# Performance work log

Hardware: AMD Instinct MI355X
Metric: run time of the kernel (lower is better)

The kernel has to match this reference:

```python
import jax, jax.numpy as jnp
import numpy as np

LN_EPS = 1e-5

def _ln(x, g, b):
    # LayerNorm over last dim; torch normalized_shape=[1,H] on [B,1,H] reduces to this
    mu = jnp.mean(x, axis=-1, keepdims=True)
    var = jnp.var(x, axis=-1, keepdims=True)
    return (x - mu) * jax.lax.rsqrt(var + LN_EPS) * g + b


def setup_inputs() -> dict:
    key = jax.random.key(0)
    B, T, D, H = 32, 2048, 512, 128
    ks = jax.random.split(key, 10)
    stdu = 1.0 / np.sqrt(H)
    u = lambda k, sh: jax.random.uniform(k, sh, jnp.float32, -stdu, stdu)
    return {
        "x": jax.random.normal(ks[0], (B, T, D), jnp.float32),
        "W_f": u(ks[1], (D, H)), "W_i": u(ks[2], (D, H)),
        "W_o": u(ks[3], (D, H)), "W_c": u(ks[4], (D, H)),
        "U_f": u(ks[5], (H, H)), "U_i": u(ks[6], (H, H)),
        "U_o": u(ks[7], (H, H)), "U_c": u(ks[8], (H, H)),
        "b_f": jnp.ones((H,), jnp.float32),
        "b_i": jnp.zeros((H,), jnp.float32),
        "b_o": jnp.zeros((H,), jnp.float32),
        "b_c": jnp.zeros((H,), jnp.float32),
        "ln_f_g": jnp.ones((H,), jnp.float32), "ln_f_b": jnp.zeros((H,), jnp.float32),
        "ln_i_g": jnp.ones((H,), jnp.float32), "ln_i_b": jnp.zeros((H,), jnp.float32),
        "ln_o_g": jnp.ones((H,), jnp.float32), "ln_o_b": jnp.zeros((H,), jnp.float32),
        "ln_c_g": jnp.ones((H,), jnp.float32), "ln_c_b": jnp.zeros((H,), jnp.float32),
        "h0": jnp.zeros((B, H), jnp.float32),
        "c0": jnp.zeros((B, H), jnp.float32),
        "zoneout_mask": jax.random.randint(ks[9], (T,), 0, 2, jnp.int32),
    }


def reference(x, W_f, W_i, W_o, W_c, U_f, U_i, U_o, U_c,
              b_f, b_i, b_o, b_c,
              ln_f_g, ln_f_b, ln_i_g, ln_i_b, ln_o_g, ln_o_b, ln_c_g, ln_c_b,
              h0, c0, zoneout_mask):
    xs = jnp.swapaxes(x, 0, 1)                       # [T, B, D]
    m = zoneout_mask.astype(x.dtype)[:, None, None]  # [T, 1, 1] zoneout indicator

    def step(carry, inp):
        h, c = carry
        x_t, mt = inp
        f = jax.nn.sigmoid(_ln(x_t @ W_f + h @ U_f + b_f, ln_f_g, ln_f_b))
        i = jax.nn.sigmoid(_ln(x_t @ W_i + h @ U_i + b_i, ln_i_g, ln_i_b))
        o = jax.nn.sigmoid(_ln(x_t @ W_o + h @ U_o + b_o, ln_o_g, ln_o_b))
        ch = jax.nn.sigmoid(_ln(x_t @ W_c + h @ U_c + b_c, ln_c_g, ln_c_b))
        c_new = mt * c + (1.0 - mt) * (f * c + i * ch)
        # NOTE: source applies sigmoid (not tanh) to the cell state
        h_new = mt * h + (1.0 - mt) * (o * jax.nn.sigmoid(c_new))
        return (h_new, c_new), h_new

    (h_T, c_T), out_seq = jax.lax.scan(step, (h0, c0), (xs, m))
    return jnp.swapaxes(out_seq, 0, 1), h_T          # [B, T, H], [B, H]
```

## Files before the change

### kernel.cpp

```cpp
#include <hip/hip_runtime.h>
#include <hip/hip_bf16.h>

#define Bx 32
#define Tt 2048
#define Dd 512
#define Hh 128

typedef __attribute__((ext_vector_type(8))) short short8;
typedef __attribute__((ext_vector_type(4))) float f32x4;

static __device__ __forceinline__ short f2bf(float f) {
    __hip_bfloat16 h = __float2bfloat16(f);
    return *reinterpret_cast<short*>(&h);
}
static __device__ __forceinline__ float sigm(float x) {
    return 1.f / (1.f + __expf(-x));
}

template<int CTRL>
static __device__ __forceinline__ float dpp_add(float v) {
    return v + __int_as_float(__builtin_amdgcn_update_dpp(
        0, __float_as_int(v), CTRL, 0xF, 0xF, true));
}
static __device__ __forceinline__ float swz_xor16_add(float v) {
    return v + __int_as_float(__builtin_amdgcn_ds_swizzle(__float_as_int(v), 0x401F));
}

#define BARRIER_LGKM() asm volatile("s_waitcnt lgkmcnt(0)\n\ts_barrier" ::: "memory")

typedef __attribute__((address_space(1))) const void gas_void;
typedef __attribute__((address_space(3))) void las_void;
static __device__ __forceinline__ void gl_lds16(const float* g, float* l) {
    __builtin_amdgcn_global_load_lds((gas_void*)g, (las_void*)l, 16, 0, 0);
}

__global__ __launch_bounds__(512, 2) void gemm_xw_mfma(
    const float* __restrict__ X,
    const float* __restrict__ W0, const float* __restrict__ W1,
    const float* __restrict__ W2, const float* __restrict__ W3,
    float* __restrict__ G)
{
    __shared__ __align__(16) short As[128][40];
    __shared__ __align__(16) short Bs[512][40];

    const int tid  = threadIdx.x;
    const int m0   = blockIdx.x * 128;
    const int lane = tid & 63;
    const int w    = tid >> 6;
    const int wr   = w >> 2, wc = w & 3;
    const int l15  = lane & 15, kb = lane >> 4;

    const int bn   = tid;
    const int gate = bn >> 7;
    const int j    = bn & 127;
    const float* __restrict__ Wg = (gate == 0) ? W0 : (gate == 1) ? W1 : (gate == 2) ? W2 : W3;

    const int am = tid >> 2;
    const int ak = (tid & 3) * 8;

    f32x4 acc[4][8];
    #pragma unroll
    for (int mt = 0; mt < 4; ++mt)
        #pragma unroll
        for (int nt = 0; nt < 8; ++nt)
            acc[mt][nt] = (f32x4){0.f, 0.f, 0.f, 0.f};

    for (int k0 = 0; k0 < Dd; k0 += 32) {
        {
            const float4* xp = (const float4*)&X[(size_t)(m0 + am) * Dd + k0 + ak];
            float4 v0 = xp[0], v1 = xp[1];
            short8 s;
            s[0] = f2bf(v0.x); s[1] = f2bf(v0.y); s[2] = f2bf(v0.z); s[3] = f2bf(v0.w);
            s[4] = f2bf(v1.x); s[5] = f2bf(v1.y); s[6] = f2bf(v1.z); s[7] = f2bf(v1.w);
            *(short8*)&As[am][ak] = s;
        }
        #pragma unroll
        for (int rc = 0; rc < 4; ++rc) {
            float v[8];
            #pragma unroll
            for (int r = 0; r < 8; ++r)
                v[r] = Wg[(size_t)(k0 + rc * 8 + r) * Hh + j];
            short8 s;
            #pragma unroll
            for (int r = 0; r < 8; ++r) s[r] = f2bf(v[r]);
            *(short8*)&Bs[bn][rc * 8] = s;
        }
        __syncthreads();

        short8 a[4], b[8];
        #pragma unroll
        for (int mt = 0; mt < 4; ++mt)
            a[mt] = *(const short8*)&As[wr * 64 + mt * 16 + l15][kb * 8];
        #pragma unroll
        for (int nt = 0; nt < 8; ++nt)
            b[nt] = *(const short8*)&Bs[wc * 128 + nt * 16 + l15][kb * 8];
        #pragma unroll
        for (int mt = 0; mt < 4; ++mt)
            #pragma unroll
            for (int nt = 0; nt < 8; ++nt)
                acc[mt][nt] = __builtin_amdgcn_mfma_f32_16x16x32_bf16(a[mt], b[nt], acc[mt][nt], 0, 0, 0);
        __syncthreads();
    }

    #pragma unroll
    for (int mt = 0; mt < 4; ++mt)
        #pragma unroll
        for (int nt = 0; nt < 8; ++nt)
            #pragma unroll
            for (int r = 0; r < 4; ++r)
                G[(size_t)(m0 + wr * 64 + mt * 16 + kb * 4 + r) * 512 + wc * 128 + nt * 16 + l15]
                    = acc[mt][nt][r];
}

__global__ __launch_bounds__(512, 1) void lstm_scan_mfma(
    const float* __restrict__ G,
    const float* __restrict__ Uf, const float* __restrict__ Ui,
    const float* __restrict__ Uo, const float* __restrict__ Uc,
    const float* __restrict__ bf_, const float* __restrict__ bi_,
    const float* __restrict__ bo_, const float* __restrict__ bc_,
    const float* __restrict__ lnfg, const float* __restrict__ lnfb,
    const float* __restrict__ lnig, const float* __restrict__ lnib,
    const float* __restrict__ lnog, const float* __restrict__ lnob,
    const float* __restrict__ lncg, const float* __restrict__ lncb,
    const float* __restrict__ h0, const float* __restrict__ c0,
    const int* __restrict__ zmask,
    float* __restrict__ out, float* __restrict__ hT)
{
    const int tid  = threadIdx.x;
    const int lane = tid & 63;
    const int w    = tid >> 6;
    const int b0   = blockIdx.x * 4;

    __shared__ __align__(16) short Ap[16 * 136];
    __shared__ __align__(16) float ST[512 * 10];
    __shared__ __align__(16) float Pan[2 * 4 * 4 * 512];
    __shared__ unsigned short act[Tt];
    __shared__ int wsum[8], wpre[8];
    __shared__ int nact_sh;

    const int gate = w >> 1;
    const float* __restrict__ Ug = (gate == 0) ? Uf : (gate == 1) ? Ui : (gate == 2) ? Uo : Uc;
    const int n0  = w * 64;
    const int l15 = lane & 15;
    const int kb  = lane >> 4;

    short8 bfr[4][4];
    #pragma unroll
    for (int nt = 0; nt < 4; ++nt) {
        const int jloc = (n0 & 127) + nt * 16 + l15;
        #pragma unroll
        for (int ks = 0; ks < 4; ++ks) {
            short8 v;
            #pragma unroll
            for (int r = 0; r < 8; ++r)
                v[r] = f2bf(Ug[(ks * 32 + kb * 8 + r) * Hh + jloc]);
            bfr[nt][ks] = v;
        }
    }

    const int rowL = tid >> 5;
    const int bL   = rowL >> 2;
    const int gL   = rowL & 3;
    const int cl   = tid & 31;
    const float* lnGp = (gL == 0) ? lnfg : (gL == 1) ? lnig : (gL == 2) ? lnog : lncg;
    const float* lnBp = (gL == 0) ? lnfb : (gL == 1) ? lnib : (gL == 2) ? lnob : lncb;
    const float* bgp  = (gL == 0) ? bf_  : (gL == 1) ? bi_  : (gL == 2) ? bo_  : bc_;
    float lgam[4], lbet[4], lbias[4];
    #pragma unroll
    for (int kk = 0; kk < 4; ++kk) {
        const int jc = cl + 32 * kk;
        lgam[kk] = lnGp[jc]; lbet[kk] = lnBp[jc]; lbias[kk] = bgp[jc];
    }

    const int ob = tid >> 7;
    const int oj = tid & 127;
    float hval = h0[(b0 + ob) * Hh + oj];
    float cval = c0[(b0 + ob) * Hh + oj];

    for (int i = tid; i < 16 * 136; i += 512) Ap[i] = 0;
    __syncthreads();
    Ap[ob * 136 + oj] = f2bf(hval);

    {
        const int base_t = tid * 4;
        const int f0 = (zmask[base_t] == 0), f1 = (zmask[base_t + 1] == 0);
        const int f2 = (zmask[base_t + 2] == 0), f3 = (zmask[base_t + 3] == 0);
        const int cnt = f0 + f1 + f2 + f3;
        int scan = cnt;
        #pragma unroll
        for (int off = 1; off <= 32; off <<= 1) {
            int v = __shfl_up(scan, off);
            if (lane >= off) scan += v;
        }
        if (lane == 63) wsum[w] = scan;
        __syncthreads();
        if (tid == 0) {
            int s = 0;
            #pragma unroll
            for (int i = 0; i < 8; ++i) { wpre[i] = s; s += wsum[i]; }
            nact_sh = s;
        }
        __syncthreads();
        int pos = wpre[w] + scan - cnt;
        if (f0) act[pos++] = (unsigned short)(base_t);
        if (f1) act[pos++] = (unsigned short)(base_t + 1);
        if (f2) act[pos++] = (unsigned short)(base_t + 2);
        if (f3) act[pos++] = (unsigned short)(base_t + 3);
    }
    __syncthreads();
    const int nact = nact_sh;

    auto stage_panel = [&](int kp, int buf) {
        #pragma unroll
        for (int si = 0; si < 2; ++si) {
            const int s    = w * 2 + si;
            const int slot = s >> 2;
            const int bb   = s & 3;
            const int kidx = kp + slot;
            if (kidx < nact) {
                const int tt = (int)act[kidx];
                const float* src = &G[((size_t)(b0 + bb) * Tt + tt) * 512];
                float* dst = &Pan[((buf * 4 + slot) * 4 + bb) * 512];
                gl_lds16(src + lane * 4, dst);
                gl_lds16(src + 256 + lane * 4, dst + 256);
            }
        }
    };

    int cur = 0;
    stage_panel(0, 0);
    asm volatile("s_waitcnt vmcnt(0)" ::: "memory");
    __syncthreads();

    auto lstm_step = [&](int kidx, int slot) {
        const int t_ = (int)act[kidx];

        float Gv[4][4];
        #pragma unroll
        for (int nt = 0; nt < 4; ++nt)
            #pragma unroll
            for (int r = 0; r < 4; ++r)
                Gv[nt][r] = Pan[((cur * 4 + slot) * 4 + r) * 512 + n0 + nt * 16 + l15];

        short8 a0 = *(const short8*)&Ap[l15 * 136 +  0 + kb * 8];
        short8 a1 = *(const short8*)&Ap[l15 * 136 + 32 + kb * 8];
        short8 a2 = *(const short8*)&Ap[l15 * 136 + 64 + kb * 8];
        short8 a3 = *(const short8*)&Ap[l15 * 136 + 96 + kb * 8];

        f32x4 C0 = {Gv[0][0], Gv[0][1], Gv[0][2], Gv[0][3]};
        f32x4 C1 = {Gv[1][0], Gv[1][1], Gv[1][2], Gv[1][3]};
        f32x4 C2 = {Gv[2][0], Gv[2][1], Gv[2][2], Gv[2][3]};
        f32x4 C3 = {Gv[3][0], Gv[3][1], Gv[3][2], Gv[3][3]};

        C0 = __builtin_amdgcn_mfma_f32_16x16x32_bf16(a0, bfr[0][0], C0, 0, 0, 0);
        C1 = __builtin_amdgcn_mfma_f32_16x16x32_bf16(a0, bfr[1][0], C1, 0, 0, 0);
        C2 = __builtin_amdgcn_mfma_f32_16x16x32_bf16(a0, bfr[2][0], C2, 0, 0, 0);
        C3 = __builtin_amdgcn_mfma_f32_16x16x32_bf16(a0, bfr[3][0], C3, 0, 0, 0);
        C0 = __builtin_amdgcn_mfma_f32_16x16x32_bf16(a1, bfr[0][1], C0, 0, 0, 0);
        C1 = __builtin_amdgcn_mfma_f32_16x16x32_bf16(a1, bfr[1][1], C1, 0, 0, 0);
        C2 = __builtin_amdgcn_mfma_f32_16x16x32_bf16(a1, bfr[2][1], C2, 0, 0, 0);
        C3 = __builtin_amdgcn_mfma_f32_16x16x32_bf16(a1, bfr[3][1], C3, 0, 0, 0);
        C0 = __builtin_amdgcn_mfma_f32_16x16x32_bf16(a2, bfr[0][2], C0, 0, 0, 0);
        C1 = __builtin_amdgcn_mfma_f32_16x16x32_bf16(a2, bfr[1][2], C1, 0, 0, 0);
        C2 = __builtin_amdgcn_mfma_f32_16x16x32_bf16(a2, bfr[2][2], C2, 0, 0, 0);
        C3 = __builtin_amdgcn_mfma_f32_16x16x32_bf16(a2, bfr[3][2], C3, 0, 0, 0);
        C0 = __builtin_amdgcn_mfma_f32_16x16x32_bf16(a3, bfr[0][3], C0, 0, 0, 0);
        C1 = __builtin_amdgcn_mfma_f32_16x16x32_bf16(a3, bfr[1][3], C1, 0, 0, 0);
        C2 = __builtin_amdgcn_mfma_f32_16x16x32_bf16(a3, bfr[2][3], C2, 0, 0, 0);
        C3 = __builtin_amdgcn_mfma_f32_16x16x32_bf16(a3, bfr[3][3], C3, 0, 0, 0);

        if (lane < 16) {
            *(float2*)&ST[(n0 +  0 + l15) * 10]     = make_float2(C0[0], C0[1]);
            *(float2*)&ST[(n0 +  0 + l15) * 10 + 2] = make_float2(C0[2], C0[3]);
            *(float2*)&ST[(n0 + 16 + l15) * 10]     = make_float2(C1[0], C1[1]);
            *(float2*)&ST[(n0 + 16 + l15) * 10 + 2] = make_float2(C1[2], C1[3]);
            *(float2*)&ST[(n0 + 32 + l15) * 10]     = make_float2(C2[0], C2[1]);
            *(float2*)&ST[(n0 + 32 + l15) * 10 + 2] = make_float2(C2[2], C2[3]);
            *(float2*)&ST[(n0 + 48 + l15) * 10]     = make_float2(C3[0], C3[1]);
            *(float2*)&ST[(n0 + 48 + l15) * 10 + 2] = make_float2(C3[2], C3[3]);
        }
        BARRIER_LGKM();

        float s0_ = ST[(gL * 128 + cl +  0) * 10 + bL] + lbias[0];
        float s1_ = ST[(gL * 128 + cl + 32) * 10 + bL] + lbias[1];
        float s2_ = ST[(gL * 128 + cl + 64) * 10 + bL] + lbias[2];
        float s3_ = ST[(gL * 128 + cl + 96) * 10 + bL] + lbias[3];
        float sm = (s0_ + s1_) + (s2_ + s3_);
        float sq = s0_ * s0_ + s1_ * s1_ + s2_ * s2_ + s3_ * s3_;
        sm = dpp_add<0xB1>(sm);  sq = dpp_add<0xB1>(sq);
        sm = dpp_add<0x4E>(sm);  sq = dpp_add<0x4E>(sq);
        sm = dpp_add<0x124>(sm); sq = dpp_add<0x124>(sq);
        sm = dpp_add<0x128>(sm); sq = dpp_add<0x128>(sq);
        sm = swz_xor16_add(sm);  sq = swz_xor16_add(sq);
        const float mu   = sm * (1.f / 128.f);
        const float rstd = rsqrtf(sq * (1.f / 128.f) - mu * mu + 1e-5f);
        ST[(gL * 128 + cl +  0) * 10 + bL] = sigm((s0_ - mu) * rstd * lgam[0] + lbet[0]);
        ST[(gL * 128 + cl + 32) * 10 + bL] = sigm((s1_ - mu) * rstd * lgam[1] + lbet[1]);
        ST[(gL * 128 + cl + 64) * 10 + bL] = sigm((s2_ - mu) * rstd * lgam[2] + lbet[2]);
        ST[(gL * 128 + cl + 96) * 10 + bL] = sigm((s3_ - mu) * rstd * lgam[3] + lbet[3]);
        BARRIER_LGKM();

        const float gf  = ST[(0   + oj) * 10 + ob];
        const float gi  = ST[(128 + oj) * 10 + ob];
        const float go  = ST[(256 + oj) * 10 + ob];
        const float gch = ST[(384 + oj) * 10 + ob];
        cval = gf * cval + gi * gch;
        hval = go * sigm(cval);
        Ap[ob * 136 + oj] = f2bf(hval);
        out[((size_t)(b0 + ob) * Tt + t_) * Hh + oj] = hval;
    };

    for (int kp = 0; kp < nact; kp += 4) {
        stage_panel(kp + 4, cur ^ 1);
        const int lim = (nact - kp < 4) ? (nact - kp) : 4;
        #pragma unroll
        for (int sl = 0; sl < 4; ++sl) {
            if (sl < lim) {
                lstm_step(kp + sl, sl);
                if (sl == 3)
                    asm volatile("s_waitcnt vmcnt(0)" ::: "memory");
                BARRIER_LGKM();
            }
        }
        cur ^= 1;
    }

    hT[(b0 + ob) * Hh + oj] = hval;
}

__global__ __launch_bounds__(512) void fill_zoneout(
    const int* __restrict__ zmask, const float* __restrict__ h0,
    float* __restrict__ out)
{
    const int t = blockIdx.x;
    if (zmask[t] == 0) return;
    int s = t - 1;
    while (s >= 0 && zmask[s] != 0) --s;
    const int tid = threadIdx.x;
    for (int idx = tid; idx < Bx * Hh; idx += 512) {
        const int b = idx >> 7, j = idx & 127;
        const float v = (s >= 0) ? out[((size_t)b * Tt + s) * Hh + j]
                                 : h0[b * Hh + j];
        out[((size_t)b * Tt + t) * Hh + j] = v;
    }
}

extern "C" void kernel_launch(void* const* d_in, const int* in_sizes, int n_in,
                              void* d_out, int out_size, void* d_ws, size_t ws_size,
                              hipStream_t stream)
{
    const float* x   = (const float*)d_in[0];
    const float* W_f = (const float*)d_in[1];
    const float* W_i = (const float*)d_in[2];
    const float* W_o = (const float*)d_in[3];
    const float* W_c = (const float*)d_in[4];
    const float* U_f = (const float*)d_in[5];
    const float* U_i = (const float*)d_in[6];
    const float* U_o = (const float*)d_in[7];
    const float* U_c = (const float*)d_in[8];
    const float* b_f = (const float*)d_in[9];
    const float* b_i = (const float*)d_in[10];
    const float* b_o = (const float*)d_in[11];
    const float* b_c = (const float*)d_in[12];
    const float* ln_f_g = (const float*)d_in[13];
    const float* ln_f_b = (const float*)d_in[14];
    const float* ln_i_g = (const float*)d_in[15];
    const float* ln_i_b = (const float*)d_in[16];
    const float* ln_o_g = (const float*)d_in[17];
    const float* ln_o_b = (const float*)d_in[18];
    const float* ln_c_g = (const float*)d_in[19];
    const float* ln_c_b = (const float*)d_in[20];
    const float* h0  = (const float*)d_in[21];
    const float* c0  = (const float*)d_in[22];
    const int*   zm  = (const int*)d_in[23];

    float* out = (float*)d_out;
    float* hT  = out + (size_t)Bx * Tt * Hh;
    float* G   = (float*)d_ws;

    gemm_xw_mfma<<<(Bx * Tt) / 128, 512, 0, stream>>>(x, W_f, W_i, W_o, W_c, G);

    lstm_scan_mfma<<<8, 512, 0, stream>>>(G, U_f, U_i, U_o, U_c,
                                          b_f, b_i, b_o, b_c,
                                          ln_f_g, ln_f_b, ln_i_g, ln_i_b,
                                          ln_o_g, ln_o_b, ln_c_g, ln_c_b,
                                          h0, c0, zm, out, hT);

    fill_zoneout<<<Tt, 512, 0, stream>>>(zm, h0, out);
}
```

Measured before the change: 1.651 ms.

## Fuse LayerNorm stats into MFMA epilogue and drop one barrier per step

Each wave now adds the precomputed input projection and bias to its MFMA results in registers, computes partial sums and sums of squares per batch row with DPP row reductions, and publishes them to a small shared array. The output threads then combine the per-wave partials, compute mean and rstd, and apply LayerNorm, sigmoid and the cell update directly. This removes the separate LayerNorm pass and one block barrier from every serial recurrence step. In exchange, each output thread does four sigmoid/LN evaluations instead of one, and the variance formulation is unchanged.

Measured after the change: 2.003 ms. 21.3% more time.

```diff
diff --git a/kernel.cpp b/kernel.cpp
--- a/kernel.cpp
+++ b/kernel.cpp
@@ -22,8 +22,12 @@
     return v + __int_as_float(__builtin_amdgcn_update_dpp(
         0, __float_as_int(v), CTRL, 0xF, 0xF, true));
 }
-static __device__ __forceinline__ float swz_xor16_add(float v) {
-    return v + __int_as_float(__builtin_amdgcn_ds_swizzle(__float_as_int(v), 0x401F));
+static __device__ __forceinline__ float rowred16(float v) {
+    v = dpp_add<0xB1>(v);
+    v = dpp_add<0x4E>(v);
+    v = dpp_add<0x124>(v);
+    v = dpp_add<0x128>(v);
+    return v;
 }
 
 #define BARRIER_LGKM() asm volatile("s_waitcnt lgkmcnt(0)\n\ts_barrier" ::: "memory")
@@ -133,6 +137,7 @@
 
     __shared__ __align__(16) short Ap[16 * 136];
     __shared__ __align__(16) float ST[512 * 10];
+    __shared__ __align__(16) float2 SQr[4][8];
     __shared__ __align__(16) float Pan[2 * 4 * 4 * 512];
     __shared__ unsigned short act[Tt];
     __shared__ int wsum[8], wpre[8];
@@ -158,22 +163,19 @@
         }
     }
 
-    const int rowL = tid >> 5;
-    const int bL   = rowL >> 2;
-    const int gL   = rowL & 3;
-    const int cl   = tid & 31;
-    const float* lnGp = (gL == 0) ? lnfg : (gL == 1) ? lnig : (gL == 2) ? lnog : lncg;
-    const float* lnBp = (gL == 0) ? lnfb : (gL == 1) ? lnib : (gL == 2) ? lnob : lncb;
-    const float* bgp  = (gL == 0) ? bf_  : (gL == 1) ? bi_  : (gL == 2) ? bo_  : bc_;
-    float lgam[4], lbet[4], lbias[4];
+    const float* __restrict__ bgA = (gate == 0) ? bf_ : (gate == 1) ? bi_ : (gate == 2) ? bo_ : bc_;
+    float biasA[4];
     #pragma unroll
-    for (int kk = 0; kk < 4; ++kk) {
-        const int jc = cl + 32 * kk;
-        lgam[kk] = lnGp[jc]; lbet[kk] = lnBp[jc]; lbias[kk] = bgp[jc];
-    }
+    for (int nt = 0; nt < 4; ++nt)
+        biasA[nt] = bgA[(n0 & 127) + nt * 16 + l15];
 
     const int ob = tid >> 7;
     const int oj = tid & 127;
+    const float gamF = lnfg[oj], betF = lnfb[oj];
+    const float gamI = lnig[oj], betI = lnib[oj];
+    const float gamO = lnog[oj], betO = lnob[oj];
+    const float gamC = lncg[oj], betC = lncb[oj];
+
     float hval = h0[(b0 + ob) * Hh + oj];
     float cval = c0[(b0 + ob) * Hh + oj];
 
@@ -247,11 +249,7 @@
         short8 a2 = *(const short8*)&Ap[l15 * 136 + 64 + kb * 8];
         short8 a3 = *(const short8*)&Ap[l15 * 136 + 96 + kb * 8];
 
-        f32x4 C0 = {Gv[0][0], Gv[0][1], Gv[0][2], Gv[0][3]};
-        f32x4 C1 = {Gv[1][0], Gv[1][1], Gv[1][2], Gv[1][3]};
-        f32x4 C2 = {Gv[2][0], Gv[2][1], Gv[2][2], Gv[2][3]};
-        f32x4 C3 = {Gv[3][0], Gv[3][1], Gv[3][2], Gv[3][3]};
-
+        f32x4 C0 = {0.f, 0.f, 0.f, 0.f}, C1 = C0, C2 = C0, C3 = C0;
         C0 = __builtin_amdgcn_mfma_f32_16x16x32_bf16(a0, bfr[0][0], C0, 0, 0, 0);
         C1 = __builtin_amdgcn_mfma_f32_16x16x32_bf16(a0, bfr[1][0], C1, 0, 0, 0);
         C2 = __builtin_amdgcn_mfma_f32_16x16x32_bf16(a0, bfr[2][0], C2, 0, 0, 0);
@@ -269,41 +267,63 @@
         C2 = __builtin_amdgcn_mfma_f32_16x16x32_bf16(a3, bfr[2][3], C2, 0, 0, 0);
         C3 = __builtin_amdgcn_mfma_f32_16x16x32_bf16(a3, bfr[3][3], C3, 0, 0, 0);
 
+        f32x4 s0, s1, s2, s3;
+        #pragma unroll
+        for (int r = 0; r < 4; ++r) {
+            s0[r] = C0[r] + Gv[0][r] + biasA[0];
+            s1[r] = C1[r] + Gv[1][r] + biasA[1];
+            s2[r] = C2[r] + Gv[2][r] + biasA[2];
+            s3[r] = C3[r] + Gv[3][r] + biasA[3];
+        }
+
+        float ps0 = s0[0] + s1[0] + s2[0] + s3[0];
+        float ps1 = s0[1] + s1[1] + s2[1] + s3[1];
+        float ps2 = s0[2] + s1[2] + s2[2] + s3[2];
+        float ps3 = s0[3] + s1[3] + s2[3] + s3[3];
+        float pq0 = s0[0]*s0[0] + s1[0]*s1[0] + s2[0]*s2[0] + s3[0]*s3[0];
+        float pq1 = s0[1]*s0[1] + s1[1]*s1[1] + s2[1]*s2[1] + s3[1]*s3[1];
+        float pq2 = s0[2]*s0[2] + s1[2]*s1[2] + s2[2]*s2[2] + s3[2]*s3[2];
+        float pq3 = s0[3]*s0[3] + s1[3]*s1[3] + s2[3]*s2[3] + s3[3]*s3[3];
+        ps0 = rowred16(ps0); ps1 = rowred16(ps1); ps2 = rowred16(ps2); ps3 = rowred16(ps3);
+        pq0 = rowred16(pq0); pq1 = rowred16(pq1); pq2 = rowred16(pq2); pq3 = rowred16(pq3);
+
         if (lane < 16) {
-            *(float2*)&ST[(n0 +  0 + l15) * 10]     = make_float2(C0[0], C0[1]);
-            *(float2*)&ST[(n0 +  0 + l15) * 10 + 2] = make_float2(C0[2], C0[3]);
-            *(float2*)&ST[(n0 + 16 + l15) * 10]     = make_float2(C1[0], C1[1]);
-            *(float2*)&ST[(n0 + 16 + l15) * 10 + 2] = make_float2(C1[2], C1[3]);
-            *(float2*)&ST[(n0 + 32 + l15) * 10]     = make_float2(C2[0], C2[1]);
-            *(float2*)&ST[(n0 + 32 + l15) * 10 + 2] = make_float2(C2[2], C2[3]);
-            *(float2*)&ST[(n0 + 48 + l15) * 10]     = make_float2(C3[0], C3[1]);
-            *(float2*)&ST[(n0 + 48 + l15) * 10 + 2] = make_float2(C3[2], C3[3]);
+            #pragma unroll
+            for (int nt = 0; nt < 4; ++nt) {
+                const int col = n0 + nt * 16 + l15;
+                const f32x4& sv = (nt == 0) ? s0 : (nt == 1) ? s1 : (nt == 2) ? s2 : s3;
+                *(float2*)&ST[col * 10]     = make_float2(sv[0], sv[1]);
+                *(float2*)&ST[col * 10 + 2] = make_float2(sv[2], sv[3]);
+            }
+        }
+        if (lane == 0) {
+            SQr[0][w] = make_float2(ps0, pq0);
+            SQr[1][w] = make_float2(ps1, pq1);
+            SQr[2][w] = make_float2(ps2, pq2);
+            SQr[3][w] = make_float2(ps3, pq3);
         }
         BARRIER_LGKM();
 
-        float s0_ = ST[(gL * 128 + cl +  0) * 10 + bL] + lbias[0];
-        float s1_ = ST[(gL * 128 + cl + 32) * 10 + bL] + lbias[1];
-        float s2_ = ST[(gL * 128 + cl + 64) * 10 + bL] + lbias[2];
-        float s3_ = ST[(gL * 128 + cl + 96) * 10 + bL] + lbias[3];
-        float sm = (s0_ + s1_) + (s2_ + s3_);
-        float sq = s0_ * s0_ + s1_ * s1_ + s2_ * s2_ + s3_ * s3_;
-        sm = dpp_add<0xB1>(sm);  sq = dpp_add<0xB1>(sq);
-        sm = dpp_add<0x4E>(sm);  sq = dpp_add<0x4E>(sq);
-        sm = dpp_add<0x124>(sm); sq = dpp_add<0x124>(sq);
-        sm = dpp_add<0x128>(sm); sq = dpp_add<0x128>(sq);
-        sm = swz_xor16_add(sm);  sq = swz_xor16_add(sq);
-        const float mu   = sm * (1.f / 128.f);
-        const float rstd = rsqrtf(sq * (1.f / 128.f) - mu * mu + 1e-5f);
-        ST[(gL * 128 + cl +  0) * 10 + bL] = sigm((s0_ - mu) * rstd * lgam[0] + lbet[0]);
-        ST[(gL * 128 + cl + 32) * 10 + bL] = sigm((s1_ - mu) * rstd * lgam[1] + lbet[1]);
-        ST[(gL * 128 + cl + 64) * 10 + bL] = sigm((s2_ - mu) * rstd * lgam[2] + lbet[2]);
-        ST[(gL * 128 + cl + 96) * 10 + bL] = sigm((s3_ - mu) * rstd * lgam[3] + lbet[3]);
-        BARRIER_LGKM();
-
-        const float gf  = ST[(0   + oj) * 10 + ob];
-        const float gi  = ST[(128 + oj) * 10 + ob];
-        const float go  = ST[(256 + oj) * 10 + ob];
-        const float gch = ST[(384 + oj) * 10 + ob];
+        const float sF = ST[(0   + oj) * 10 + ob];
+        const float sI = ST[(128 + oj) * 10 + ob];
+        const float sO = ST[(256 + oj) * 10 + ob];
+        const float sC = ST[(384 + oj) * 10 + ob];
+        f32x4 q01 = *(const f32x4*)&SQr[ob][0];
+        f32x4 q23 = *(const f32x4*)&SQr[ob][2];
+        f32x4 q45 = *(const f32x4*)&SQr[ob][4];
+        f32x4 q67 = *(const f32x4*)&SQr[ob][6];
+        const float SF = q01[0] + q01[2], QF = q01[1] + q01[3];
+        const float SI = q23[0] + q23[2], QI = q23[1] + q23[3];
+        const float SO = q45[0] + q45[2], QO = q45[1] + q45[3];
+        const float SC = q67[0] + q67[2], QC = q67[1] + q67[3];
+        const float muF = SF * (1.f/128.f), rF = rsqrtf(QF*(1.f/128.f) - muF*muF + 1e-5f);
+        const float muI = SI * (1.f/128.f), rI = rsqrtf(QI*(1.f/128.f) - muI*muI + 1e-5f);
+        const float muO = SO * (1.f/128.f), rO = rsqrtf(QO*(1.f/128.f) - muO*muO + 1e-5f);
+        const float muC = SC * (1.f/128.f), rC = rsqrtf(QC*(1.f/128.f) - muC*muC + 1e-5f);
+        const float gf  = sigm((sF - muF) * rF * gamF + betF);
+        const float gi  = sigm((sI - muI) * rI * gamI + betI);
+        const float go  = sigm((sO - muO) * rO * gamO + betO);
+        const float gch = sigm((sC - muC) * rC * gamC + betC);
         cval = gf * cval + gi * gch;
         hval = go * sigm(cval);
         Ap[ob * 136 + oj] = f2bf(hval);
```
